# Kernel tuning notes

Hardware: AMD Instinct MI355X
Metric: run time of the kernel (lower is better)

## Reference

```python
import jax, jax.numpy as jnp
import numpy as np

N, DIM = 1024, 3
DEPTH, H1, H2, NF = 4, 64, 32, 8
L = 1.0
PI = np.pi


def _h2_features(x):
    n, dim = x.shape
    rij = x[:, None, :] - x[None, :, :]                       # (n, n, dim)
    eye = jnp.eye(n, dtype=x.dtype)
    # distance of periodic sine displacement, diagonal regularized then zeroed
    r = jnp.linalg.norm(jnp.sin(PI * rij / L) + eye[..., None], axis=-1) * (1.0 - eye)
    kf = jnp.arange(1, NF + 1, dtype=x.dtype)                 # (NF,)
    ang = (2.0 * PI / L) * rij[:, :, None, :] * kf[:, None]   # (n, n, NF, dim)
    # original concat order per frequency k: cos block (dim cols) then sin block
    cs = jnp.stack([jnp.cos(ang), jnp.sin(ang)], axis=3)      # (n, n, NF, 2, dim)
    return jnp.concatenate([r[..., None], cs.reshape(n, n, 2 * NF * dim)], axis=-1)


def _h1_init(t, n):
    t = jnp.reshape(t, ())
    kf = jnp.arange(1, NF + 1, dtype=jnp.float32)
    ang = 2.0 * PI * t * kf                                   # (NF,)
    feats = jnp.concatenate([t[None], jnp.stack([jnp.cos(ang), jnp.sin(ang)], axis=1).reshape(-1)])
    return jnp.broadcast_to(feats[None, :], (n, 1 + 2 * NF))  # (n, 17)


def _combine(h1, h2):
    n = h1.shape[0]
    g2 = jnp.mean(h2, axis=0)                                 # (n, h2f)
    g1 = jnp.broadcast_to(jnp.mean(h1, axis=0, keepdims=True), h1.shape)
    return jnp.concatenate([h1, g1, g2], axis=1)


def _forward(x, t, W1, b1, W2, b2, Wf):
    n, dim = x.shape
    h1 = _h1_init(t, n)
    h2 = _h2_features(x)
    for d in range(DEPTH - 1):
        f = _combine(h1, h2)
        h1u = jnp.tanh(f @ W1[d] + b1[d])
        h2u = jnp.tanh(h2 @ W2[d] + b2[d])
        h1 = h1u + h1 if d > 0 else h1u
        h2 = h2u + h2 if d > 0 else h2u
    f = _combine(h1, h2)
    h1 = jnp.tanh(f @ W1[-1] + b1[-1]) + h1
    force = jnp.clip(2.0 * x, -10.0, 10.0)
    return -(h1 @ Wf) * force


def setup_inputs():
    key = jax.random.key(0)
    ks = jax.random.split(key, 20)
    s = 0.01
    inp = {
        "x": jax.random.normal(ks[0], (N, DIM), jnp.float32),
        "t": jax.random.uniform(ks[1], (), dtype=jnp.float32),
    }
    f0 = 2 * (1 + 2 * NF) + (1 + 2 * NF * DIM)  # 83
    fl = 2 * H1 + H2                            # 160
    w1_in = [f0, fl, fl, fl]
    w2_in = [1 + 2 * NF * DIM, H2, H2]
    for d in range(DEPTH):
        inp[f"W1_{d}"] = s * jax.random.normal(ks[2 + d], (w1_in[d], H1), jnp.float32)
        inp[f"b1_{d}"] = jnp.zeros((H1,), jnp.float32)
    for d in range(DEPTH - 1):
        inp[f"W2_{d}"] = s * jax.random.normal(ks[8 + d], (w2_in[d], H2), jnp.float32)
        inp[f"b2_{d}"] = jnp.zeros((H2,), jnp.float32)
    inp["Wf"] = s * jax.random.normal(ks[15], (H1, DIM), jnp.float32)
    return inp


def reference(x, t, W1_0, b1_0, W1_1, b1_1, W1_2, b1_2, W1_3, b1_3,
              W2_0, b2_0, W2_1, b2_1, W2_2, b2_2, Wf):
    W1 = [W1_0, W1_1, W1_2, W1_3]
    b1 = [b1_0, b1_1, b1_2, b1_3]
    W2 = [W2_0, W2_1, W2_2]
    b2 = [b2_0, b2_1, b2_2]
    return _forward(x, t, W1, b1, W2, b2, Wf)
```

## Files before the change

kernel.cpp:

```cpp
#include <hip/hip_runtime.h>
#include <math.h>


#define NP 1024

static const size_t OF_TROW = 0;
static const size_t OF_CSUM = OF_TROW + NP*56;
static const size_t OF_SSUM = OF_CSUM + 24;
static const size_t OF_HSUM = OF_SSUM + 24;
static const size_t OF_RACC = OF_HSUM + 192;
static const size_t OF_M0   = OF_RACC + NP;
static const size_t OF_M1   = OF_M0 + NP*32;
static const size_t OF_M2   = OF_M1 + NP*32;
static const size_t OF_H1A  = OF_M2 + NP*32;
static const size_t OF_H1B  = OF_H1A + NP*64;

__device__ __forceinline__ float ftanh(float x) {
    float e = __expf(2.0f * x);
    return 1.0f - __fdividef(2.0f, e + 1.0f);
}

__global__ __launch_bounds__(1024) void k1_tables(
    const float* __restrict__ X,
    float* __restrict__ TROW,
    float* __restrict__ CSUM, float* __restrict__ SSUM,
    float* __restrict__ HSUM)
{
    const int i = threadIdx.x;
    float ck[24], sk[24], cp[3], sp[3];
#pragma unroll
    for (int d = 0; d < 3; ++d) {
        float x = X[i*3 + d];
        sincospif(x, &sp[d], &cp[d]);
#pragma unroll
        for (int k = 0; k < 8; ++k) {
            float s, c;
            sincospif(2.0f*(float)(k+1)*x, &s, &c);
            ck[k*3 + d] = c;  sk[k*3 + d] = s;
        }
    }
    float4* row = (float4*)(TROW + (size_t)i*56);
#pragma unroll
    for (int t = 0; t < 12; ++t)
        row[t] = make_float4(ck[2*t], sk[2*t], ck[2*t+1], sk[2*t+1]);
    row[12] = make_float4(cp[0], sp[0], cp[1], sp[1]);
    row[13] = make_float4(cp[2], sp[2], 0.f, 0.f);

    __shared__ float part[48*16];
    const int lane = i & 63, wv = i >> 6;
#pragma unroll
    for (int v = 0; v < 24; ++v) {
        float a = ck[v], b = sk[v];
#pragma unroll
        for (int off = 32; off; off >>= 1) {
            a += __shfl_down(a, off, 64);
            b += __shfl_down(b, off, 64);
        }
        if (lane == 0) { part[v*16 + wv] = a; part[(24+v)*16 + wv] = b; }
    }
    __syncthreads();
    if (i < 48) {
        float s = 0.f;
#pragma unroll
        for (int w = 0; w < 16; ++w) s += part[i*16 + w];
        if (i < 24) CSUM[i] = s; else SSUM[i-24] = s;
    }
    if (i < 192) HSUM[i] = 0.0f;
}

__global__ __launch_bounds__(512, 4) void k2_pairs(
    const float* __restrict__ W20, const float* __restrict__ b20,
    const float* __restrict__ W21, const float* __restrict__ b21,
    const float* __restrict__ W22, const float* __restrict__ b22,
    const float* __restrict__ TROW,
    float* __restrict__ RACC, float* __restrict__ M0,
    float* __restrict__ M1, float* __restrict__ M2)
{
    __shared__ __align__(16) float sH0[128*32];
    __shared__ __align__(16) float sH1[128*32];
    __shared__ __align__(16) float sJ[56];

    const int tid  = threadIdx.x;
    const int lane = tid & 63;
    const int wid  = __builtin_amdgcn_readfirstlane(tid >> 6);
    const int c0   = wid * 4;
    const int j    = blockIdx.x;
    const int lx   = lane & 7;

    if (tid < 14) ((float4*)sJ)[tid] = ((const float4*)(TROW + (size_t)j*56))[tid];

    const float b0x = b20[c0+0], b0y = b20[c0+1], b0z = b20[c0+2], b0w = b20[c0+3];
    const float b1x = b21[c0+0], b1y = b21[c0+1], b1z = b21[c0+2], b1w = b21[c0+3];
    const float b2x = b22[c0+0], b2y = b22[c0+1], b2z = b22[c0+2], b2w = b22[c0+3];
    __syncthreads();

    float4* H0a = (float4*)sH0 + lane*8;
    float4* H0b = (float4*)sH0 + (lane+64)*8;
    float4* H1a = (float4*)sH1 + lane*8;
    float4* H1b = (float4*)sH1 + (lane+64)*8;

    float a0x=0.f,a0y=0.f,a0z=0.f,a0w=0.f;
    float a1x=0.f,a1y=0.f,a1z=0.f,a1w=0.f;
    float a2x=0.f,a2y=0.f,a2z=0.f,a2w=0.f;
    float racc = 0.f;

#pragma unroll 1
    for (int tile = 0; tile < 8; ++tile) {
        const float4* rowA = (const float4*)(TROW + (size_t)(tile*128 + lane)*56);
        const float4* rowB = rowA + 14*64;

        float rA, rB;
        {
            const float4 pa = rowA[12], pb = rowA[13];
            float s0 = fmaf(pa.y, sJ[48], -(pa.x * sJ[49]));
            float s1 = fmaf(pa.w, sJ[50], -(pa.z * sJ[51]));
            float s2 = fmaf(pb.y, sJ[52], -(pb.x * sJ[53]));
            rA = sqrtf(fmaf(s0, s0, fmaf(s1, s1, s2*s2)));
        }
        {
            const float4 pa = rowB[12], pb = rowB[13];
            float s0 = fmaf(pa.y, sJ[48], -(pa.x * sJ[49]));
            float s1 = fmaf(pa.w, sJ[50], -(pa.z * sJ[51]));
            float s2 = fmaf(pb.y, sJ[52], -(pb.x * sJ[53]));
            rB = sqrtf(fmaf(s0, s0, fmaf(s1, s1, s2*s2)));
        }
        racc += rA + rB;

        float zA0, zA1, zA2, zA3, zB0, zB1, zB2, zB3;
        {
            const float* w = W20 + c0;
            zA0 = fmaf(rA, w[0], b0x); zA1 = fmaf(rA, w[1], b0y);
            zA2 = fmaf(rA, w[2], b0z); zA3 = fmaf(rA, w[3], b0w);
            zB0 = fmaf(rB, w[0], b0x); zB1 = fmaf(rB, w[1], b0y);
            zB2 = fmaf(rB, w[2], b0z); zB3 = fmaf(rB, w[3], b0w);
        }
#pragma unroll
        for (int t = 0; t < 12; ++t) {
            const float4 fA = rowA[t], fB = rowB[t];
#pragma unroll
            for (int sub = 0; sub < 2; ++sub) {
                const int kd = 2*t + sub;
                const int k = kd/3, d = kd - k*3;
                const float cj = sJ[2*kd], sj = sJ[2*kd+1];
                const float* wc = W20 + (1 + k*6 + d)*32 + c0;
                const float* ws = W20 + (4 + k*6 + d)*32 + c0;
                const float ciA = sub ? fA.z : fA.x, siA = sub ? fA.w : fA.y;
                const float ciB = sub ? fB.z : fB.x, siB = sub ? fB.w : fB.y;
                const float ccA = fmaf(ciA, cj, siA*sj);
                const float ssA = fmaf(siA, cj, -(ciA*sj));
                const float ccB = fmaf(ciB, cj, siB*sj);
                const float ssB = fmaf(siB, cj, -(ciB*sj));
                zA0 = fmaf(ccA, wc[0], fmaf(ssA, ws[0], zA0));
                zA1 = fmaf(ccA, wc[1], fmaf(ssA, ws[1], zA1));
                zA2 = fmaf(ccA, wc[2], fmaf(ssA, ws[2], zA2));
                zA3 = fmaf(ccA, wc[3], fmaf(ssA, ws[3], zA3));
                zB0 = fmaf(ccB, wc[0], fmaf(ssB, ws[0], zB0));
                zB1 = fmaf(ccB, wc[1], fmaf(ssB, ws[1], zB1));
                zB2 = fmaf(ccB, wc[2], fmaf(ssB, ws[2], zB2));
                zB3 = fmaf(ccB, wc[3], fmaf(ssB, ws[3], zB3));
            }
        }

        float hA0 = ftanh(zA0), hA1 = ftanh(zA1), hA2 = ftanh(zA2), hA3 = ftanh(zA3);
        float hB0 = ftanh(zB0), hB1 = ftanh(zB1), hB2 = ftanh(zB2), hB3 = ftanh(zB3);
        a0x += hA0 + hB0; a0y += hA1 + hB1; a0z += hA2 + hB2; a0w += hA3 + hB3;
        H0a[wid ^ lx] = make_float4(hA0, hA1, hA2, hA3);
        H0b[wid ^ lx] = make_float4(hB0, hB1, hB2, hB3);
        __syncthreads();

        zA0 = b1x; zA1 = b1y; zA2 = b1z; zA3 = b1w;
        zB0 = b1x; zB1 = b1y; zB2 = b1z; zB3 = b1w;
#pragma unroll
        for (int kc = 0; kc < 8; ++kc) {
            const float4 hA = H0a[kc ^ lx];
            const float4 hB = H0b[kc ^ lx];
            const float* w0 = W21 + (kc*4+0)*32 + c0;
            const float* w1 = W21 + (kc*4+1)*32 + c0;
            const float* w2 = W21 + (kc*4+2)*32 + c0;
            const float* w3 = W21 + (kc*4+3)*32 + c0;
            zA0 = fmaf(hA.x,w0[0], fmaf(hA.y,w1[0], fmaf(hA.z,w2[0], fmaf(hA.w,w3[0], zA0))));
            zA1 = fmaf(hA.x,w0[1], fmaf(hA.y,w1[1], fmaf(hA.z,w2[1], fmaf(hA.w,w3[1], zA1))));
            zA2 = fmaf(hA.x,w0[2], fmaf(hA.y,w1[2], fmaf(hA.z,w2[2], fmaf(hA.w,w3[2], zA2))));
            zA3 = fmaf(hA.x,w0[3], fmaf(hA.y,w1[3], fmaf(hA.z,w2[3], fmaf(hA.w,w3[3], zA3))));
            zB0 = fmaf(hB.x,w0[0], fmaf(hB.y,w1[0], fmaf(hB.z,w2[0], fmaf(hB.w,w3[0], zB0))));
            zB1 = fmaf(hB.x,w0[1], fmaf(hB.y,w1[1], fmaf(hB.z,w2[1], fmaf(hB.w,w3[1], zB1))));
            zB2 = fmaf(hB.x,w0[2], fmaf(hB.y,w1[2], fmaf(hB.z,w2[2], fmaf(hB.w,w3[2], zB2))));
            zB3 = fmaf(hB.x,w0[3], fmaf(hB.y,w1[3], fmaf(hB.z,w2[3], fmaf(hB.w,w3[3], zB3))));
        }
        hA0 = ftanh(zA0) + hA0; hA1 = ftanh(zA1) + hA1;
        hA2 = ftanh(zA2) + hA2; hA3 = ftanh(zA3) + hA3;
        hB0 = ftanh(zB0) + hB0; hB1 = ftanh(zB1) + hB1;
        hB2 = ftanh(zB2) + hB2; hB3 = ftanh(zB3) + hB3;
        a1x += hA0 + hB0; a1y += hA1 + hB1; a1z += hA2 + hB2; a1w += hA3 + hB3;
        H1a[wid ^ lx] = make_float4(hA0, hA1, hA2, hA3);
        H1b[wid ^ lx] = make_float4(hB0, hB1, hB2, hB3);
        __syncthreads();

        zA0 = b2x; zA1 = b2y; zA2 = b2z; zA3 = b2w;
        zB0 = b2x; zB1 = b2y; zB2 = b2z; zB3 = b2w;
#pragma unroll
        for (int kc = 0; kc < 8; ++kc) {
            const float4 hA = H1a[kc ^ lx];
            const float4 hB = H1b[kc ^ lx];
            const float* w0 = W22 + (kc*4+0)*32 + c0;
            const float* w1 = W22 + (kc*4+1)*32 + c0;
            const float* w2 = W22 + (kc*4+2)*32 + c0;
            const float* w3 = W22 + (kc*4+3)*32 + c0;
            zA0 = fmaf(hA.x,w0[0], fmaf(hA.y,w1[0], fmaf(hA.z,w2[0], fmaf(hA.w,w3[0], zA0))));
            zA1 = fmaf(hA.x,w0[1], fmaf(hA.y,w1[1], fmaf(hA.z,w2[1], fmaf(hA.w,w3[1], zA1))));
            zA2 = fmaf(hA.x,w0[2], fmaf(hA.y,w1[2], fmaf(hA.z,w2[2], fmaf(hA.w,w3[2], zA2))));
            zA3 = fmaf(hA.x,w0[3], fmaf(hA.y,w1[3], fmaf(hA.z,w2[3], fmaf(hA.w,w3[3], zA3))));
            zB0 = fmaf(hB.x,w0[0], fmaf(hB.y,w1[0], fmaf(hB.z,w2[0], fmaf(hB.w,w3[0], zB0))));
            zB1 = fmaf(hB.x,w0[1], fmaf(hB.y,w1[1], fmaf(hB.z,w2[1], fmaf(hB.w,w3[1], zB1))));
            zB2 = fmaf(hB.x,w0[2], fmaf(hB.y,w1[2], fmaf(hB.z,w2[2], fmaf(hB.w,w3[2], zB2))));
            zB3 = fmaf(hB.x,w0[3], fmaf(hB.y,w1[3], fmaf(hB.z,w2[3], fmaf(hB.w,w3[3], zB3))));
        }
        a2x += ftanh(zA0) + hA0 + ftanh(zB0) + hB0;
        a2y += ftanh(zA1) + hA1 + ftanh(zB1) + hB1;
        a2z += ftanh(zA2) + hA2 + ftanh(zB2) + hB2;
        a2w += ftanh(zA3) + hA3 + ftanh(zB3) + hB3;
    }

#pragma unroll
    for (int mask = 1; mask < 64; mask <<= 1) {
        a0x += __shfl_xor(a0x, mask, 64); a0y += __shfl_xor(a0y, mask, 64);
        a0z += __shfl_xor(a0z, mask, 64); a0w += __shfl_xor(a0w, mask, 64);
        a1x += __shfl_xor(a1x, mask, 64); a1y += __shfl_xor(a1y, mask, 64);
        a1z += __shfl_xor(a1z, mask, 64); a1w += __shfl_xor(a1w, mask, 64);
        a2x += __shfl_xor(a2x, mask, 64); a2y += __shfl_xor(a2y, mask, 64);
        a2z += __shfl_xor(a2z, mask, 64); a2w += __shfl_xor(a2w, mask, 64);
        racc += __shfl_xor(racc, mask, 64);
    }
    if (lane == 0) {
        *(float4*)(M0 + j*32 + c0) = make_float4(a0x, a0y, a0z, a0w);
        *(float4*)(M1 + j*32 + c0) = make_float4(a1x, a1y, a1z, a1w);
        *(float4*)(M2 + j*32 + c0) = make_float4(a2x, a2y, a2z, a2w);
        if (wid == 0) RACC[j] = racc;
    }
}

#define FMA8(fv, wptr) do { \
    const float4* w4_ = (const float4*)(wptr); \
    float4 a_ = w4_[0], b_ = w4_[1]; \
    z[0]=fmaf((fv),a_.x,z[0]); z[1]=fmaf((fv),a_.y,z[1]); \
    z[2]=fmaf((fv),a_.z,z[2]); z[3]=fmaf((fv),a_.w,z[3]); \
    z[4]=fmaf((fv),b_.x,z[4]); z[5]=fmaf((fv),b_.y,z[5]); \
    z[6]=fmaf((fv),b_.z,z[6]); z[7]=fmaf((fv),b_.w,z[7]); \
} while (0)

__device__ __forceinline__ void hsum_atomic(float* HS, const float h[8],
                                            int tid, int c0) {
    float hs[8];
#pragma unroll
    for (int u = 0; u < 8; ++u) {
        hs[u] = h[u];
#pragma unroll
        for (int mask = 8; mask < 64; mask <<= 1)
            hs[u] += __shfl_xor(hs[u], mask, 64);
    }
    if (((tid & 63) >> 3) == 0) {
#pragma unroll
        for (int u = 0; u < 8; ++u) atomicAdd(&HS[c0 + u], hs[u]);
    }
}

__global__ __launch_bounds__(256) void l0_kernel(
    const float* __restrict__ Tsc, const float* __restrict__ W10,
    const float* __restrict__ b10,
    const float* __restrict__ TROW,
    const float* __restrict__ CSUM, const float* __restrict__ SSUM,
    const float* __restrict__ RACC,
    float* __restrict__ H1A, float* __restrict__ HSUM0)
{
    const int tid = threadIdx.x;
    const int gid = blockIdx.x*256 + tid;
    const int j = gid >> 3, qq = gid & 7, c0 = qq*8;
    const float inv_n = 1.0f/1024.0f;
    const float t = Tsc[0];

    float z[8];
#pragma unroll
    for (int u = 0; u < 8; ++u) z[u] = b10[c0+u];

    FMA8(t, W10 + 0*64 + c0);
    FMA8(t, W10 + 17*64 + c0);
#pragma unroll
    for (int k = 0; k < 8; ++k) {
        float s, c; sincospif(2.0f*(float)(k+1)*t, &s, &c);
        FMA8(c, W10 + (1+2*k)*64 + c0);
        FMA8(c, W10 + (18+2*k)*64 + c0);
        FMA8(s, W10 + (2+2*k)*64 + c0);
        FMA8(s, W10 + (19+2*k)*64 + c0);
    }
    {
        float rb = RACC[j] * inv_n;
        FMA8(rb, W10 + 34*64 + c0);
    }
    const float4* rj = (const float4*)(TROW + (size_t)j*56);
#pragma unroll
    for (int tt = 0; tt < 12; ++tt) {
        float4 v = rj[tt];
#pragma unroll
        for (int sub = 0; sub < 2; ++sub) {
            const int kd = 2*tt + sub;
            float cj = sub ? v.z : v.x;
            float sj = sub ? v.w : v.y;
            float Cb = CSUM[kd]*inv_n, Sb = SSUM[kd]*inv_n;
            float cm = fmaf(cj, Cb, sj*Sb);
            float sm = fmaf(Sb, cj, -(Cb*sj));
            int k = kd/3, d = kd - k*3;
            FMA8(cm, W10 + (35 + k*6 + d)*64 + c0);
            FMA8(sm, W10 + (38 + k*6 + d)*64 + c0);
        }
    }
    float h[8];
#pragma unroll
    for (int u = 0; u < 8; ++u) {
        h[u] = ftanh(z[u]);
        H1A[j*64 + c0 + u] = h[u];
    }
    hsum_atomic(HSUM0, h, tid, c0);
}

template<int LAYER>
__global__ __launch_bounds__(256) void lx_kernel(
    const float* __restrict__ W, const float* __restrict__ b,
    const float* __restrict__ hin, float* __restrict__ hout,
    const float* __restrict__ HSin, float* __restrict__ HSout,
    const float* __restrict__ M,
    const float* __restrict__ Wf, const float* __restrict__ X,
    float* __restrict__ out)
{
    const int tid = threadIdx.x;
    const int gid = blockIdx.x*256 + tid;
    const int j = gid >> 3, qq = gid & 7, c0 = qq*8;
    const float inv_n = 1.0f/1024.0f;

    float z[8];
#pragma unroll
    for (int u = 0; u < 8; ++u) z[u] = b[c0+u];
    const float* hrow = hin + j*64;
#pragma unroll 4
    for (int p = 0; p < 64; ++p) FMA8(hrow[p], W + p*64 + c0);
#pragma unroll 4
    for (int p = 0; p < 64; ++p) FMA8(HSin[p]*inv_n, W + (64+p)*64 + c0);
    const float* mrow = M + j*32;
#pragma unroll 4
    for (int p = 0; p < 32; ++p) FMA8(mrow[p]*inv_n, W + (128+p)*64 + c0);
    float h[8];
#pragma unroll
    for (int u = 0; u < 8; ++u) h[u] = ftanh(z[u]) + hrow[c0+u];

    if (LAYER < 3) {
#pragma unroll
        for (int u = 0; u < 8; ++u) hout[j*64 + c0 + u] = h[u];
        hsum_atomic(HSout, h, tid, c0);
    } else {
        __shared__ float red[256][3];
        float p0 = 0.f, p1 = 0.f, p2 = 0.f;
#pragma unroll
        for (int u = 0; u < 8; ++u) {
            float hv = h[u];
            const float* wf = Wf + (c0+u)*3;
            p0 = fmaf(hv, wf[0], p0);
            p1 = fmaf(hv, wf[1], p1);
            p2 = fmaf(hv, wf[2], p2);
        }
        red[tid][0] = p0; red[tid][1] = p1; red[tid][2] = p2;
        __syncthreads();
        if (qq == 0) {
            float s0 = 0.f, s1 = 0.f, s2 = 0.f;
#pragma unroll
            for (int r = 0; r < 8; ++r) {
                s0 += red[tid+r][0]; s1 += red[tid+r][1]; s2 += red[tid+r][2];
            }
#pragma unroll
            for (int d = 0; d < 3; ++d) {
                float fx = 2.0f * X[j*3 + d];
                fx = fminf(fmaxf(fx, -10.0f), 10.0f);
                float s = (d == 0 ? s0 : (d == 1 ? s1 : s2));
                out[j*3 + d] = -s * fx;
            }
        }
    }
}

extern "C" void kernel_launch(void* const* d_in, const int* in_sizes, int n_in,
                              void* d_out, int out_size, void* d_ws, size_t ws_size,
                              hipStream_t stream)
{
    const float* X   = (const float*)d_in[0];
    const float* Tsc = (const float*)d_in[1];
    const float* W10 = (const float*)d_in[2];  const float* b10 = (const float*)d_in[3];
    const float* W11 = (const float*)d_in[4];  const float* b11 = (const float*)d_in[5];
    const float* W12 = (const float*)d_in[6];  const float* b12 = (const float*)d_in[7];
    const float* W13 = (const float*)d_in[8];  const float* b13 = (const float*)d_in[9];
    const float* W20 = (const float*)d_in[10]; const float* b20 = (const float*)d_in[11];
    const float* W21 = (const float*)d_in[12]; const float* b21 = (const float*)d_in[13];
    const float* W22 = (const float*)d_in[14]; const float* b22 = (const float*)d_in[15];
    const float* Wf  = (const float*)d_in[16];

    float* ws  = (float*)d_ws;
    float* out = (float*)d_out;

    float* TROW = ws + OF_TROW;
    float* CSUM = ws + OF_CSUM; float* SSUM = ws + OF_SSUM;
    float* HSUM = ws + OF_HSUM; float* RACC = ws + OF_RACC;
    float* M0 = ws + OF_M0; float* M1 = ws + OF_M1; float* M2 = ws + OF_M2;
    float* H1A = ws + OF_H1A; float* H1B = ws + OF_H1B;

    k1_tables<<<1, 1024, 0, stream>>>(X, TROW, CSUM, SSUM, HSUM);
    k2_pairs<<<NP, 512, 0, stream>>>(W20, b20, W21, b21, W22, b22,
                                     TROW, RACC, M0, M1, M2);
    l0_kernel<<<32, 256, 0, stream>>>(Tsc, W10, b10, TROW, CSUM, SSUM, RACC,
                                      H1A, HSUM + 0*64);
    lx_kernel<1><<<32, 256, 0, stream>>>(W11, b11, H1A, H1B, HSUM + 0*64, HSUM + 1*64,
                                         M0, (const float*)nullptr, (const float*)nullptr,
                                         (float*)nullptr);
    lx_kernel<2><<<32, 256, 0, stream>>>(W12, b12, H1B, H1A, HSUM + 1*64, HSUM + 2*64,
                                         M1, (const float*)nullptr, (const float*)nullptr,
                                         (float*)nullptr);
    lx_kernel<3><<<32, 256, 0, stream>>>(W13, b13, H1A, H1B, HSUM + 2*64, (float*)nullptr,
                                         M2, Wf, X, out);
}
```

Measured before the change: 458.8 us.

## Precompute per-j weight products in pair kernel and fuse h1 layers with grid sync

In the pair kernel, each block now folds the j-row cos/sin values into the first W2 layer weights once, stored in shared memory. The inner loop then does two FMAs per output instead of recomputing angle-difference products and reading global weights. Separately, the four h1 layer kernels are merged into one persistent 64-block kernel. h1 rows stay in shared memory, and layers are separated by an atomic-counter grid barrier, which removes three launches and the global h1 round trips. The barrier assumes all 64 blocks are resident at once, and it replaces the final shared-memory reduction with shuffles.

```diff
diff --git a/kernel.cpp b/kernel.cpp
--- a/kernel.cpp
+++ b/kernel.cpp
@@ -8,12 +8,11 @@
 static const size_t OF_CSUM = OF_TROW + NP*56;
 static const size_t OF_SSUM = OF_CSUM + 24;
 static const size_t OF_HSUM = OF_SSUM + 24;
-static const size_t OF_RACC = OF_HSUM + 192;
+static const size_t OF_CNT  = OF_HSUM + 192;
+static const size_t OF_RACC = OF_CNT + 4;
 static const size_t OF_M0   = OF_RACC + NP;
 static const size_t OF_M1   = OF_M0 + NP*32;
 static const size_t OF_M2   = OF_M1 + NP*32;
-static const size_t OF_H1A  = OF_M2 + NP*32;
-static const size_t OF_H1B  = OF_H1A + NP*64;
 
 __device__ __forceinline__ float ftanh(float x) {
     float e = __expf(2.0f * x);
@@ -24,7 +23,7 @@
     const float* __restrict__ X,
     float* __restrict__ TROW,
     float* __restrict__ CSUM, float* __restrict__ SSUM,
-    float* __restrict__ HSUM)
+    float* __restrict__ HSUM, int* __restrict__ CNT)
 {
     const int i = threadIdx.x;
     float ck[24], sk[24], cp[3], sp[3];
@@ -66,6 +65,7 @@
         if (i < 24) CSUM[i] = s; else SSUM[i-24] = s;
     }
     if (i < 192) HSUM[i] = 0.0f;
+    if (i == 200) CNT[0] = 0;
 }
 
 __global__ __launch_bounds__(512, 4) void k2_pairs(
@@ -79,6 +79,7 @@
     __shared__ __align__(16) float sH0[128*32];
     __shared__ __align__(16) float sH1[128*32];
     __shared__ __align__(16) float sJ[56];
+    __shared__ __align__(16) float sPQ[24*64];
 
     const int tid  = threadIdx.x;
     const int lane = tid & 63;
@@ -92,6 +93,19 @@
     const float b0x = b20[c0+0], b0y = b20[c0+1], b0z = b20[c0+2], b0w = b20[c0+3];
     const float b1x = b21[c0+0], b1y = b21[c0+1], b1z = b21[c0+2], b1w = b21[c0+3];
     const float b2x = b22[c0+0], b2y = b22[c0+1], b2z = b22[c0+2], b2w = b22[c0+3];
+    __syncthreads();
+
+    for (int idx = tid; idx < 24*64; idx += 512) {
+        const int kd = idx >> 6;
+        const int e  = idx & 63;
+        const int c  = e & 31;
+        const int k = kd/3, d = kd - k*3;
+        const float wcv = W20[(1 + k*6 + d)*32 + c];
+        const float wsv = W20[(4 + k*6 + d)*32 + c];
+        const float cj = sJ[2*kd], sj = sJ[2*kd+1];
+        sPQ[idx] = (e < 32) ? fmaf(cj, wcv, -(sj*wsv))
+                            : fmaf(sj, wcv,   cj*wsv);
+    }
     __syncthreads();
 
     float4* H0a = (float4*)sH0 + lane*8;
@@ -140,24 +154,18 @@
 #pragma unroll
             for (int sub = 0; sub < 2; ++sub) {
                 const int kd = 2*t + sub;
-                const int k = kd/3, d = kd - k*3;
-                const float cj = sJ[2*kd], sj = sJ[2*kd+1];
-                const float* wc = W20 + (1 + k*6 + d)*32 + c0;
-                const float* ws = W20 + (4 + k*6 + d)*32 + c0;
+                const float4 P = *(const float4*)(sPQ + kd*64 + c0);
+                const float4 Q = *(const float4*)(sPQ + kd*64 + 32 + c0);
                 const float ciA = sub ? fA.z : fA.x, siA = sub ? fA.w : fA.y;
                 const float ciB = sub ? fB.z : fB.x, siB = sub ? fB.w : fB.y;
-                const float ccA = fmaf(ciA, cj, siA*sj);
-                const float ssA = fmaf(siA, cj, -(ciA*sj));
-                const float ccB = fmaf(ciB, cj, siB*sj);
-                const float ssB = fmaf(siB, cj, -(ciB*sj));
-                zA0 = fmaf(ccA, wc[0], fmaf(ssA, ws[0], zA0));
-                zA1 = fmaf(ccA, wc[1], fmaf(ssA, ws[1], zA1));
-                zA2 = fmaf(ccA, wc[2], fmaf(ssA, ws[2], zA2));
-                zA3 = fmaf(ccA, wc[3], fmaf(ssA, ws[3], zA3));
-                zB0 = fmaf(ccB, wc[0], fmaf(ssB, ws[0], zB0));
-                zB1 = fmaf(ccB, wc[1], fmaf(ssB, ws[1], zB1));
-                zB2 = fmaf(ccB, wc[2], fmaf(ssB, ws[2], zB2));
-                zB3 = fmaf(ccB, wc[3], fmaf(ssB, ws[3], zB3));
+                zA0 = fmaf(ciA, P.x, fmaf(siA, Q.x, zA0));
+                zA1 = fmaf(ciA, P.y, fmaf(siA, Q.y, zA1));
+                zA2 = fmaf(ciA, P.z, fmaf(siA, Q.z, zA2));
+                zA3 = fmaf(ciA, P.w, fmaf(siA, Q.w, zA3));
+                zB0 = fmaf(ciB, P.x, fmaf(siB, Q.x, zB0));
+                zB1 = fmaf(ciB, P.y, fmaf(siB, Q.y, zB1));
+                zB2 = fmaf(ciB, P.z, fmaf(siB, Q.z, zB2));
+                zB3 = fmaf(ciB, P.w, fmaf(siB, Q.w, zB3));
             }
         }
 
@@ -248,6 +256,8 @@
     z[6]=fmaf((fv),b_.z,z[6]); z[7]=fmaf((fv),b_.w,z[7]); \
 } while (0)
 
+#define HSTR 65
+
 __device__ __forceinline__ void hsum_atomic(float* HS, const float h[8],
                                             int tid, int c0) {
     float hs[8];
@@ -264,121 +274,147 @@
     }
 }
 
-__global__ __launch_bounds__(256) void l0_kernel(
-    const float* __restrict__ Tsc, const float* __restrict__ W10,
-    const float* __restrict__ b10,
+__device__ __forceinline__ void gsync(int* cnt, int target, int tid) {
+    __syncthreads();
+    if (tid == 0) {
+        __threadfence();
+        atomicAdd(cnt, 1);
+        while (atomicAdd(cnt, 0) < target) {}
+    }
+    __syncthreads();
+}
+
+__global__ __launch_bounds__(128) void h1_all(
+    const float* __restrict__ Tsc,
+    const float* __restrict__ W10, const float* __restrict__ b10,
+    const float* __restrict__ W11, const float* __restrict__ b11,
+    const float* __restrict__ W12, const float* __restrict__ b12,
+    const float* __restrict__ W13, const float* __restrict__ b13,
+    const float* __restrict__ Wf,  const float* __restrict__ X,
     const float* __restrict__ TROW,
     const float* __restrict__ CSUM, const float* __restrict__ SSUM,
     const float* __restrict__ RACC,
-    float* __restrict__ H1A, float* __restrict__ HSUM0)
-{
-    const int tid = threadIdx.x;
-    const int gid = blockIdx.x*256 + tid;
-    const int j = gid >> 3, qq = gid & 7, c0 = qq*8;
-    const float inv_n = 1.0f/1024.0f;
-    const float t = Tsc[0];
-
-    float z[8];
-#pragma unroll
-    for (int u = 0; u < 8; ++u) z[u] = b10[c0+u];
-
-    FMA8(t, W10 + 0*64 + c0);
-    FMA8(t, W10 + 17*64 + c0);
-#pragma unroll
-    for (int k = 0; k < 8; ++k) {
-        float s, c; sincospif(2.0f*(float)(k+1)*t, &s, &c);
-        FMA8(c, W10 + (1+2*k)*64 + c0);
-        FMA8(c, W10 + (18+2*k)*64 + c0);
-        FMA8(s, W10 + (2+2*k)*64 + c0);
-        FMA8(s, W10 + (19+2*k)*64 + c0);
-    }
-    {
-        float rb = RACC[j] * inv_n;
-        FMA8(rb, W10 + 34*64 + c0);
-    }
-    const float4* rj = (const float4*)(TROW + (size_t)j*56);
-#pragma unroll
-    for (int tt = 0; tt < 12; ++tt) {
-        float4 v = rj[tt];
-#pragma unroll
-        for (int sub = 0; sub < 2; ++sub) {
-            const int kd = 2*tt + sub;
-            float cj = sub ? v.z : v.x;
-            float sj = sub ? v.w : v.y;
-            float Cb = CSUM[kd]*inv_n, Sb = SSUM[kd]*inv_n;
-            float cm = fmaf(cj, Cb, sj*Sb);
-            float sm = fmaf(Sb, cj, -(Cb*sj));
-            int k = kd/3, d = kd - k*3;
-            FMA8(cm, W10 + (35 + k*6 + d)*64 + c0);
-            FMA8(sm, W10 + (38 + k*6 + d)*64 + c0);
-        }
-    }
-    float h[8];
-#pragma unroll
-    for (int u = 0; u < 8; ++u) {
-        h[u] = ftanh(z[u]);
-        H1A[j*64 + c0 + u] = h[u];
-    }
-    hsum_atomic(HSUM0, h, tid, c0);
-}
-
-template<int LAYER>
-__global__ __launch_bounds__(256) void lx_kernel(
-    const float* __restrict__ W, const float* __restrict__ b,
-    const float* __restrict__ hin, float* __restrict__ hout,
-    const float* __restrict__ HSin, float* __restrict__ HSout,
-    const float* __restrict__ M,
-    const float* __restrict__ Wf, const float* __restrict__ X,
+    const float* __restrict__ M0, const float* __restrict__ M1,
+    const float* __restrict__ M2,
+    float* __restrict__ HSUM, int* __restrict__ CNT,
     float* __restrict__ out)
 {
+    __shared__ float sH[16*HSTR];
+    __shared__ float sG[64];
     const int tid = threadIdx.x;
-    const int gid = blockIdx.x*256 + tid;
+    const int gid = blockIdx.x*128 + tid;
     const int j = gid >> 3, qq = gid & 7, c0 = qq*8;
+    const int lj = tid >> 3;
     const float inv_n = 1.0f/1024.0f;
-
-    float z[8];
-#pragma unroll
-    for (int u = 0; u < 8; ++u) z[u] = b[c0+u];
-    const float* hrow = hin + j*64;
-#pragma unroll 4
-    for (int p = 0; p < 64; ++p) FMA8(hrow[p], W + p*64 + c0);
-#pragma unroll 4
-    for (int p = 0; p < 64; ++p) FMA8(HSin[p]*inv_n, W + (64+p)*64 + c0);
-    const float* mrow = M + j*32;
-#pragma unroll 4
-    for (int p = 0; p < 32; ++p) FMA8(mrow[p]*inv_n, W + (128+p)*64 + c0);
+    float* myrow = sH + lj*HSTR;
+
     float h[8];
-#pragma unroll
-    for (int u = 0; u < 8; ++u) h[u] = ftanh(z[u]) + hrow[c0+u];
-
-    if (LAYER < 3) {
-#pragma unroll
-        for (int u = 0; u < 8; ++u) hout[j*64 + c0 + u] = h[u];
-        hsum_atomic(HSout, h, tid, c0);
-    } else {
-        __shared__ float red[256][3];
+    {
+        const float t = Tsc[0];
+        float z[8];
+#pragma unroll
+        for (int u = 0; u < 8; ++u) z[u] = b10[c0+u];
+        FMA8(t, W10 + 0*64 + c0);
+        FMA8(t, W10 + 17*64 + c0);
+#pragma unroll
+        for (int k = 0; k < 8; ++k) {
+            float s, c; sincospif(2.0f*(float)(k+1)*t, &s, &c);
+            FMA8(c, W10 + (1+2*k)*64 + c0);
+            FMA8(c, W10 + (18+2*k)*64 + c0);
+            FMA8(s, W10 + (2+2*k)*64 + c0);
+            FMA8(s, W10 + (19+2*k)*64 + c0);
+        }
+        FMA8(RACC[j]*inv_n, W10 + 34*64 + c0);
+        const float4* rj = (const float4*)(TROW + (size_t)j*56);
+#pragma unroll
+        for (int tt = 0; tt < 12; ++tt) {
+            float4 v = rj[tt];
+#pragma unroll
+            for (int sub = 0; sub < 2; ++sub) {
+                const int kd = 2*tt + sub;
+                float cj = sub ? v.z : v.x;
+                float sj = sub ? v.w : v.y;
+                float Cb = CSUM[kd]*inv_n, Sb = SSUM[kd]*inv_n;
+                float cm = fmaf(cj, Cb, sj*Sb);
+                float sm = fmaf(Sb, cj, -(Cb*sj));
+                int k = kd/3, d = kd - k*3;
+                FMA8(cm, W10 + (35 + k*6 + d)*64 + c0);
+                FMA8(sm, W10 + (38 + k*6 + d)*64 + c0);
+            }
+        }
+#pragma unroll
+        for (int u = 0; u < 8; ++u) {
+            h[u] = ftanh(z[u]);
+            myrow[c0+u] = h[u];
+        }
+        hsum_atomic(HSUM + 0*64, h, tid, c0);
+    }
+    gsync(CNT, 64, tid);
+    if (tid < 64) sG[tid] = __hip_atomic_load(&HSUM[0*64+tid], __ATOMIC_RELAXED,
+                                              __HIP_MEMORY_SCOPE_AGENT) * inv_n;
+    __syncthreads();
+
+#pragma unroll 1
+    for (int L = 1; L <= 2; ++L) {
+        const float* W = (L == 1) ? W11 : W12;
+        const float* b = (L == 1) ? b11 : b12;
+        const float* M = (L == 1) ? M0  : M1;
+        float z[8];
+#pragma unroll
+        for (int u = 0; u < 8; ++u) z[u] = b[c0+u];
+#pragma unroll 4
+        for (int p = 0; p < 64; ++p) FMA8(myrow[p], W + p*64 + c0);
+#pragma unroll 4
+        for (int p = 0; p < 64; ++p) FMA8(sG[p], W + (64+p)*64 + c0);
+        const float* mrow = M + j*32;
+#pragma unroll 4
+        for (int p = 0; p < 32; ++p) FMA8(mrow[p]*inv_n, W + (128+p)*64 + c0);
+#pragma unroll
+        for (int u = 0; u < 8; ++u) h[u] = ftanh(z[u]) + myrow[c0+u];
+        __syncthreads();
+#pragma unroll
+        for (int u = 0; u < 8; ++u) myrow[c0+u] = h[u];
+        hsum_atomic(HSUM + L*64, h, tid, c0);
+        gsync(CNT, 64*(L+1), tid);
+        if (tid < 64) sG[tid] = __hip_atomic_load(&HSUM[L*64+tid], __ATOMIC_RELAXED,
+                                                  __HIP_MEMORY_SCOPE_AGENT) * inv_n;
+        __syncthreads();
+    }
+
+    {
+        float z[8];
+#pragma unroll
+        for (int u = 0; u < 8; ++u) z[u] = b13[c0+u];
+#pragma unroll 4
+        for (int p = 0; p < 64; ++p) FMA8(myrow[p], W13 + p*64 + c0);
+#pragma unroll 4
+        for (int p = 0; p < 64; ++p) FMA8(sG[p], W13 + (64+p)*64 + c0);
+        const float* mrow = M2 + j*32;
+#pragma unroll 4
+        for (int p = 0; p < 32; ++p) FMA8(mrow[p]*inv_n, W13 + (128+p)*64 + c0);
+#pragma unroll
+        for (int u = 0; u < 8; ++u) h[u] = ftanh(z[u]) + myrow[c0+u];
+
         float p0 = 0.f, p1 = 0.f, p2 = 0.f;
 #pragma unroll
         for (int u = 0; u < 8; ++u) {
-            float hv = h[u];
             const float* wf = Wf + (c0+u)*3;
-            p0 = fmaf(hv, wf[0], p0);
-            p1 = fmaf(hv, wf[1], p1);
-            p2 = fmaf(hv, wf[2], p2);
-        }
-        red[tid][0] = p0; red[tid][1] = p1; red[tid][2] = p2;
-        __syncthreads();
+            p0 = fmaf(h[u], wf[0], p0);
+            p1 = fmaf(h[u], wf[1], p1);
+            p2 = fmaf(h[u], wf[2], p2);
+        }
+#pragma unroll
+        for (int m = 1; m < 8; m <<= 1) {
+            p0 += __shfl_xor(p0, m, 64);
+            p1 += __shfl_xor(p1, m, 64);
+            p2 += __shfl_xor(p2, m, 64);
+        }
         if (qq == 0) {
-            float s0 = 0.f, s1 = 0.f, s2 = 0.f;
-#pragma unroll
-            for (int r = 0; r < 8; ++r) {
-                s0 += red[tid+r][0]; s1 += red[tid+r][1]; s2 += red[tid+r][2];
-            }
 #pragma unroll
             for (int d = 0; d < 3; ++d) {
                 float fx = 2.0f * X[j*3 + d];
                 fx = fminf(fmaxf(fx, -10.0f), 10.0f);
-                float s = (d == 0 ? s0 : (d == 1 ? s1 : s2));
+                float s = (d == 0 ? p0 : (d == 1 ? p1 : p2));
                 out[j*3 + d] = -s * fx;
             }
         }
@@ -405,21 +441,14 @@
 
     float* TROW = ws + OF_TROW;
     float* CSUM = ws + OF_CSUM; float* SSUM = ws + OF_SSUM;
-    float* HSUM = ws + OF_HSUM; float* RACC = ws + OF_RACC;
+    float* HSUM = ws + OF_HSUM; int*   CNT  = (int*)(ws + OF_CNT);
+    float* RACC = ws + OF_RACC;
     float* M0 = ws + OF_M0; float* M1 = ws + OF_M1; float* M2 = ws + OF_M2;
-    float* H1A = ws + OF_H1A; float* H1B = ws + OF_H1B;
-
-    k1_tables<<<1, 1024, 0, stream>>>(X, TROW, CSUM, SSUM, HSUM);
+
+    k1_tables<<<1, 1024, 0, stream>>>(X, TROW, CSUM, SSUM, HSUM, CNT);
     k2_pairs<<<NP, 512, 0, stream>>>(W20, b20, W21, b21, W22, b22,
                                      TROW, RACC, M0, M1, M2);
-    l0_kernel<<<32, 256, 0, stream>>>(Tsc, W10, b10, TROW, CSUM, SSUM, RACC,
-                                      H1A, HSUM + 0*64);
-    lx_kernel<1><<<32, 256, 0, stream>>>(W11, b11, H1A, H1B, HSUM + 0*64, HSUM + 1*64,
-                                         M0, (const float*)nullptr, (const float*)nullptr,
-                                         (float*)nullptr);
-    lx_kernel<2><<<32, 256, 0, stream>>>(W12, b12, H1B, H1A, HSUM + 1*64, HSUM + 2*64,
-                                         M1, (const float*)nullptr, (const float*)nullptr,
-                                         (float*)nullptr);
-    lx_kernel<3><<<32, 256, 0, stream>>>(W13, b13, H1A, H1B, HSUM + 2*64, (float*)nullptr,
-                                         M2, Wf, X, out);
-}
+    h1_all<<<64, 128, 0, stream>>>(Tsc, W10, b10, W11, b11, W12, b12, W13, b13,
+                                   Wf, X, TROW, CSUM, SSUM, RACC,
+                                   M0, M1, M2, HSUM, CNT, out);
+}
```

Result: faster. 414.7 us (median of 3 runs) (-9.6%).
